# Optimization experiments

Hardware: AMD Instinct MI355X
Metric: run time of the kernel (lower is better)

The kernel has to match this reference:

```python
import jax, jax.numpy as jnp
import numpy as np

OUT_FEATURES = 4096
IN_FEATURES = 16384
NNZ = 2_000_000
BATCH = 128


def setup_inputs() -> dict:
    key = jax.random.key(0)
    k1, k2, k3, k4, k5 = jax.random.split(key, 5)
    inputs = jax.random.normal(k1, (BATCH, IN_FEATURES), dtype=jnp.float32)
    # learned sparse weight values and bias (uniform init like reset_parameters)
    bound = 1.0 / (IN_FEATURES ** 0.5)
    values = jax.random.uniform(k2, (NNZ,), minval=-bound, maxval=bound, dtype=jnp.float32)
    bias = jax.random.uniform(k3, (OUT_FEATURES,), minval=-bound, maxval=bound, dtype=jnp.float32)
    # fixed COO connectivity: rows -> out_features, cols -> in_features
    rows = jax.random.randint(k4, (NNZ,), 0, OUT_FEATURES, dtype=jnp.int32)
    cols = jax.random.randint(k5, (NNZ,), 0, IN_FEATURES, dtype=jnp.int32)
    return {"inputs": inputs, "values": values, "bias": bias, "rows": rows, "cols": cols}


def reference(inputs, values, bias, rows, cols):
    # out[b, r] = sum_{k: rows[k]==r} values[k] * inputs[b, cols[k]]  (+ bias[r])
    # Gather input columns per nnz entry, scale, then scatter-add into output rows.
    contrib = inputs[:, cols] * values            # [B, nnz]
    out = jax.ops.segment_sum(contrib.T, rows, num_segments=OUT_FEATURES).T  # [B, out_features]
    return out + bias
```

## Files before the change

kernel.cpp:

```cpp
#include <hip/hip_runtime.h>
#include <hip/hip_fp16.h>

#define NNZ    2000000
#define BATCH  128
#define IN_F   16384
#define OUT_F  4096
#define NCH    1024
#define CHUNK  1956
#define NBK    1024
#define RPB    4
#define BK_CAP 2240

__device__ inline int mbcnt64(unsigned long long m) {
  return __builtin_amdgcn_mbcnt_hi((unsigned)(m >> 32),
         __builtin_amdgcn_mbcnt_lo((unsigned)m, 0));
}

__global__ __launch_bounds__(512)
void k_localsort(const int* __restrict__ rows, const int* __restrict__ cols,
                 const float* __restrict__ vals, int* __restrict__ desc,
                 int2* __restrict__ pairs) {
  __shared__ int2 stage[CHUNK];
  __shared__ int  h[NBK], cur[NBK];
  __shared__ int  wsums[8];
  const int t = threadIdx.x, c = blockIdx.x;
  const int lane = t & 63, w = t >> 6;
  const int base = c * CHUNK;
  const int n = min(CHUNK, NNZ - base);
  const int n4 = n >> 2;

  h[t] = 0; h[t + 512] = 0;
  __syncthreads();
  for (int i = t; i < n4; i += 512) {
    const int4 r4 = ((const int4*)(rows + base))[i];
    atomicAdd(&h[r4.x >> 2], 1);
    atomicAdd(&h[r4.y >> 2], 1);
    atomicAdd(&h[r4.z >> 2], 1);
    atomicAdd(&h[r4.w >> 2], 1);
  }
  __syncthreads();
  const int v0 = h[2 * t], v1 = h[2 * t + 1];
  const int sv = v0 + v1;
  int x = sv;
#pragma unroll
  for (int off = 1; off < 64; off <<= 1) { int y = __shfl_up(x, off); if (lane >= off) x += y; }
  if (lane == 63) wsums[w] = x;
  __syncthreads();
  int wex = 0;
#pragma unroll
  for (int j = 0; j < 8; ++j) { const int sj = wsums[j]; wex += (j < w) ? sj : 0; }
  const int excl = wex + x - sv;
  cur[2 * t] = excl;
  cur[2 * t + 1] = excl + v0;
  ((int2*)desc)[c * 512 + t] = make_int2((excl << 8) | v0, ((excl + v0) << 8) | v1);
  __syncthreads();
  for (int i = t; i < n4; i += 512) {
    const int4   r4 = ((const int4*)(rows + base))[i];
    const int4   c4 = ((const int4*)(cols + base))[i];
    const float4 f4 = ((const float4*)(vals + base))[i];
    int pos;
    pos = atomicAdd(&cur[r4.x >> 2], 1); stage[pos] = make_int2((r4.x << 14) | c4.x, __float_as_int(f4.x));
    pos = atomicAdd(&cur[r4.y >> 2], 1); stage[pos] = make_int2((r4.y << 14) | c4.y, __float_as_int(f4.y));
    pos = atomicAdd(&cur[r4.z >> 2], 1); stage[pos] = make_int2((r4.z << 14) | c4.z, __float_as_int(f4.z));
    pos = atomicAdd(&cur[r4.w >> 2], 1); stage[pos] = make_int2((r4.w << 14) | c4.w, __float_as_int(f4.w));
  }
  __syncthreads();
  const int nh = n >> 1;
  for (int j = t; j < nh; j += 512)
    ((int4*)(pairs + base))[j] = ((const int4*)stage)[j];
}

__global__ __launch_bounds__(256)
void k_dtr(const int* __restrict__ desc, int* __restrict__ descT) {
  __shared__ int tile[32][33];
  const int tx = threadIdx.x, ty = threadIdx.y;
  const int x0 = blockIdx.x * 32, y0 = blockIdx.y * 32;
#pragma unroll
  for (int j = 0; j < 32; j += 8)
    tile[ty + j][tx] = desc[(y0 + ty + j) * NBK + x0 + tx];
  __syncthreads();
#pragma unroll
  for (int j = 0; j < 32; j += 8)
    descT[(x0 + ty + j) * NCH + y0 + tx] = tile[tx][ty + j];
}

__global__ __launch_bounds__(256)
void k_cscan(const int* __restrict__ descT, unsigned* __restrict__ rdesc,
             int* __restrict__ btot) {
  const int t = threadIdx.x, lane = t & 63, w = t >> 6;
  const int b = blockIdx.x * 4 + w;
  int carry = 0;
#pragma unroll
  for (int j = 0; j < 16; ++j) {
    const int cc = j * 64 + lane;
    const unsigned d = (unsigned)descT[b * NCH + cc];
    const int len = (int)(d & 255u);
    int x = len;
#pragma unroll
    for (int off = 1; off < 64; off <<= 1) { int y = __shfl_up(x, off); if (lane >= off) x += y; }
    rdesc[b * NCH + cc] = (d << 12) | (unsigned)(carry + x - len);
    carry += __shfl(x, 63);
  }
  if (lane == 0) btot[b] = carry;
}

__global__ __launch_bounds__(256)
void k_transpose(const float* __restrict__ in, __half* __restrict__ inT) {
  __shared__ float tile[32][33];
  const int tx = threadIdx.x, ty = threadIdx.y;
  const int c0 = blockIdx.x * 32, b0 = blockIdx.y * 32;
#pragma unroll
  for (int j = 0; j < 32; j += 8)
    tile[ty + j][tx] = in[(b0 + ty + j) * IN_F + c0 + tx];
  __syncthreads();
#pragma unroll
  for (int j = 0; j < 32; j += 8)
    inT[(size_t)(c0 + ty + j) * BATCH + b0 + tx] = __float2half(tile[tx][ty + j]);
}

#define REFILL(SL, KK) do { \
    const int idx = (hh_ + 2 * (KK)) * 8 + 2 * g; \
    const bool vld = idx < nr; \
    const int i0_ = vld ? (s + idx) : 0; \
    uint4 pp = *((const uint4*)(sorted + i0_)); \
    if (!vld) { pp.y = 0u; pp.w = 0u; } \
    x##SL##0 = inT[(pp.x & 16383u) * 16 + q]; \
    x##SL##1 = inT[(pp.z & 16383u) * 16 + q]; \
    pv##SL = make_uint2(pp.y, pp.w); \
  } while (0)

#define FMAH(SL) do { \
    const __half2 hv0 = __float2half2_rn(__uint_as_float(pv##SL.x)); \
    const __half2 hv1 = __float2half2_rn(__uint_as_float(pv##SL.y)); \
    const __half2* h0 = (const __half2*)&x##SL##0; \
    const __half2* h1 = (const __half2*)&x##SL##1; \
    hac0 = __hfma2(hv0, h0[0], hac0); hac1 = __hfma2(hv0, h0[1], hac1); \
    hac2 = __hfma2(hv0, h0[2], hac2); hac3 = __hfma2(hv0, h0[3], hac3); \
    hac0 = __hfma2(hv1, h1[0], hac0); hac1 = __hfma2(hv1, h1[1], hac1); \
    hac2 = __hfma2(hv1, h1[2], hac2); hac3 = __hfma2(hv1, h1[3], hac3); \
  } while (0)

#define STAGE(SL, NEXTKK) do { FMAH(SL); REFILL(SL, NEXTKK); } while (0)

#define FLUSH() do { \
    float2 f0 = __half22float2(hac0), f1 = __half22float2(hac1); \
    float2 f2 = __half22float2(hac2), f3 = __half22float2(hac3); \
    a0 += f0.x; a1 += f0.y; a2 += f1.x; a3 += f1.y; \
    a4 += f2.x; a5 += f2.y; a6 += f3.x; a7 += f3.y; \
    hac0 = hz; hac1 = hz; hac2 = hz; hac3 = hz; \
  } while (0)

__global__ __launch_bounds__(512, 8)
void k_spmm(const uint4* __restrict__ inT, const int2* __restrict__ pairs,
            const unsigned* __restrict__ rdesc, const int* __restrict__ btot,
            const float* __restrict__ bias, float* __restrict__ out) {
  __shared__ __align__(16) int2 staging[BK_CAP];
  __shared__ __align__(16) int2 sorted[BK_CAP + 8];
  __shared__ int  exd[NCH];
  __shared__ int  wrun[32];
  __shared__ unsigned long long wmask[32];
  __shared__ int  wcnt[32];
  __shared__ int  lst[RPB + 1];
  const int t = threadIdx.x, b = blockIdx.x;
  const int w = t >> 6, lane = t & 63;
  const int n = min(btot[b], BK_CAP);
  const int nrnd = (n + 511) & ~511;

  exd[t] = (int)rdesc[b * NCH + t];
  exd[t + 512] = (int)rdesc[b * NCH + t + 512];
  __syncthreads();
  for (int i = t; i < n; i += 512) {
    int lo = 0, hi = NCH - 1;
#pragma unroll
    for (int st = 0; st < 10; ++st) {
      const int mid = (lo + hi + 1) >> 1;
      if ((exd[mid] & 4095) <= i) lo = mid; else hi = mid - 1;
    }
    const unsigned d = (unsigned)exd[lo];
    staging[i] = pairs[lo * CHUNK + (int)(d >> 20) + (i - (int)(d & 4095u))];
  }
  __syncthreads();

  int cnt = 0;
  for (int i = w * 64 + lane; i < nrnd; i += 512) {
    const bool valid = i < n;
    const int key = valid ? staging[i].x : 0;
    const int r4 = valid ? ((key >> 14) & 3) : 4;
    unsigned long long m[4];
#pragma unroll
    for (int r = 0; r < 4; ++r) m[r] = __ballot(r4 == r);
    if (lane < 4) cnt += __popcll(m[lane]);
  }
  if (lane < 4) wcnt[w * 4 + lane] = cnt;
  __syncthreads();

  if (w == 0 && lane < 32) {
    const int v = wcnt[lane];
    int x = v;
#pragma unroll
    for (int off = 4; off < 32; off <<= 1) { int y = __shfl_up(x, off); if (lane >= off) x += y; }
    const int exw = x - v;
    int lstr = 0, tpad = 0;
#pragma unroll
    for (int rr = 0; rr < 4; ++rr) {
      const int tr = __shfl(x, 28 + rr);
      const int trE = (tr + 1) & ~1;
      if ((lane & 3) > rr) lstr += trE;
      tpad += trE;
    }
    wrun[lane] = lstr + exw;
    if (lane < 4) lst[lane] = lstr;
    if (lane == 0) lst[RPB] = tpad;
    if (lane >= 28) {
      if (x & 1) sorted[lstr + x] = make_int2(0, 0);
    }
  }
  __syncthreads();

  for (int i = w * 64 + lane; i < nrnd; i += 512) {
    const bool valid = i < n;
    const int2 p = valid ? staging[i] : make_int2(0, 0);
    const int r4 = valid ? ((p.x >> 14) & 3) : 4;
    unsigned long long m[4];
#pragma unroll
    for (int r = 0; r < 4; ++r) m[r] = __ballot(r4 == r);
    if (lane < 4) wmask[w * 4 + lane] = m[lane];
    if (valid) {
      const int rank = wrun[w * 4 + r4] + mbcnt64(wmask[w * 4 + r4]);
      sorted[rank] = p;
    }
    if (lane < 4) wrun[w * 4 + lane] += __popcll(m[lane]);
  }
  __syncthreads();

  const int rloc = w >> 1, hh_ = w & 1;
  const int r = b * RPB + rloc;
  const int g = lane >> 4, q = lane & 15;
  const int s = lst[rloc];
  const int nr = lst[rloc + 1] - s;
  const int nsteps = (nr + 7) >> 3;
  const int K = (nsteps + 1) >> 1;
  const int K3 = ((K + 2) / 3) * 3;

  float a0 = 0.f, a1 = 0.f, a2 = 0.f, a3 = 0.f, a4 = 0.f, a5 = 0.f, a6 = 0.f, a7 = 0.f;
  const __half2 hz = __float2half2_rn(0.f);
  __half2 hac0 = hz, hac1 = hz, hac2 = hz, hac3 = hz;
  uint4 xA0, xA1, xB0, xB1, xC0, xC1;
  uint2 pvA, pvB, pvC;

  REFILL(A, 0);
  REFILL(B, 1);
  REFILL(C, 2);
  for (int kk = 0; kk < K3; kk += 3) {
    STAGE(A, kk + 3);
    STAGE(B, kk + 4);
    STAGE(C, kk + 5);
    FLUSH();
  }

  a0 += __shfl_xor(a0, 16); a0 += __shfl_xor(a0, 32);
  a1 += __shfl_xor(a1, 16); a1 += __shfl_xor(a1, 32);
  a2 += __shfl_xor(a2, 16); a2 += __shfl_xor(a2, 32);
  a3 += __shfl_xor(a3, 16); a3 += __shfl_xor(a3, 32);
  a4 += __shfl_xor(a4, 16); a4 += __shfl_xor(a4, 32);
  a5 += __shfl_xor(a5, 16); a5 += __shfl_xor(a5, 32);
  a6 += __shfl_xor(a6, 16); a6 += __shfl_xor(a6, 32);
  a7 += __shfl_xor(a7, 16); a7 += __shfl_xor(a7, 32);

  float (*part)[BATCH] = (float (*)[BATCH])staging;
  if (hh_ == 1 && g == 0) {
    const int o = q * 8;
    part[rloc][o + 0] = a0; part[rloc][o + 1] = a1;
    part[rloc][o + 2] = a2; part[rloc][o + 3] = a3;
    part[rloc][o + 4] = a4; part[rloc][o + 5] = a5;
    part[rloc][o + 6] = a6; part[rloc][o + 7] = a7;
  }
  __syncthreads();
  if (hh_ == 0 && g == 0) {
    const float bs_ = bias[r];
    const int o = q * 8;
    out[(o + 0) * OUT_F + r] = a0 + part[rloc][o + 0] + bs_;
    out[(o + 1) * OUT_F + r] = a1 + part[rloc][o + 1] + bs_;
    out[(o + 2) * OUT_F + r] = a2 + part[rloc][o + 2] + bs_;
    out[(o + 3) * OUT_F + r] = a3 + part[rloc][o + 3] + bs_;
    out[(o + 4) * OUT_F + r] = a4 + part[rloc][o + 4] + bs_;
    out[(o + 5) * OUT_F + r] = a5 + part[rloc][o + 5] + bs_;
    out[(o + 6) * OUT_F + r] = a6 + part[rloc][o + 6] + bs_;
    out[(o + 7) * OUT_F + r] = a7 + part[rloc][o + 7] + bs_;
  }
}

extern "C" void kernel_launch(void* const* d_in, const int* in_sizes, int n_in,
                              void* d_out, int out_size, void* d_ws, size_t ws_size,
                              hipStream_t stream) {
  const float* inputs = (const float*)d_in[0];
  const float* values = (const float*)d_in[1];
  const float* bias   = (const float*)d_in[2];
  const int*   rows   = (const int*)d_in[3];
  const int*   cols   = (const int*)d_in[4];
  float* out = (float*)d_out;

  char* ws = (char*)d_ws;
  __half*   inputT = (__half*)(ws);
  int2*     pairs  = (int2*)(ws + 4194304);
  int*      desc   = (int*)(ws + 20217856);
  int*      descT  = (int*)(ws + 24412160);
  unsigned* rdesc  = (unsigned*)descT;
  int*      btot   = (int*)(ws + 28606464);

  k_localsort<<<NCH,     512, 0, stream>>>(rows, cols, values, desc, pairs);
  k_dtr      <<<dim3(NBK / 32, NCH / 32), dim3(32, 8), 0, stream>>>(desc, descT);
  k_cscan    <<<NBK / 4, 256, 0, stream>>>(descT, rdesc, btot);
  k_transpose<<<dim3(IN_F / 32, BATCH / 32), dim3(32, 8), 0, stream>>>(inputs, inputT);
  k_spmm     <<<NBK,     512, 0, stream>>>((const uint4*)inputT, pairs, rdesc, btot, bias, out);
}
```

Before: 133.9 us.

## Pack sorted nnz entries into 32-bit words with fp16 values, halve chunk count

Each sorted nonzero is packed into one 32-bit word (14-bit column, 2-bit local row, fp16 value) instead of an 8-byte pair, halving the pairs buffer traffic and LDS staging size. The chunk count drops from 1024 to 512 with doubled chunk size, shrinking the descriptor transpose/scan and the binary search depth in the spmm kernel. The value is now rounded to fp16 when written rather than when used, so the numeric result is unchanged. The layout and offsets of every kernel are rewritten to match.

```diff
diff --git a/kernel.cpp b/kernel.cpp
--- a/kernel.cpp
+++ b/kernel.cpp
@@ -5,8 +5,8 @@
 #define BATCH  128
 #define IN_F   16384
 #define OUT_F  4096
-#define NCH    1024
-#define CHUNK  1956
+#define NCH    512
+#define CHUNK  3912
 #define NBK    1024
 #define RPB    4
 #define BK_CAP 2240
@@ -16,13 +16,14 @@
          __builtin_amdgcn_mbcnt_lo((unsigned)m, 0));
 }
 
+
 __global__ __launch_bounds__(512)
 void k_localsort(const int* __restrict__ rows, const int* __restrict__ cols,
                  const float* __restrict__ vals, int* __restrict__ desc,
-                 int2* __restrict__ pairs) {
-  __shared__ int2 stage[CHUNK];
-  __shared__ int  h[NBK], cur[NBK];
-  __shared__ int  wsums[8];
+                 unsigned* __restrict__ pairs) {
+  __shared__ unsigned stage[CHUNK];
+  __shared__ int h[NBK], cur[NBK];
+  __shared__ int wsums[8];
   const int t = threadIdx.x, c = blockIdx.x;
   const int lane = t & 63, w = t >> 6;
   const int base = c * CHUNK;
@@ -59,15 +60,18 @@
     const int4   c4 = ((const int4*)(cols + base))[i];
     const float4 f4 = ((const float4*)(vals + base))[i];
     int pos;
-    pos = atomicAdd(&cur[r4.x >> 2], 1); stage[pos] = make_int2((r4.x << 14) | c4.x, __float_as_int(f4.x));
-    pos = atomicAdd(&cur[r4.y >> 2], 1); stage[pos] = make_int2((r4.y << 14) | c4.y, __float_as_int(f4.y));
-    pos = atomicAdd(&cur[r4.z >> 2], 1); stage[pos] = make_int2((r4.z << 14) | c4.z, __float_as_int(f4.z));
-    pos = atomicAdd(&cur[r4.w >> 2], 1); stage[pos] = make_int2((r4.w << 14) | c4.w, __float_as_int(f4.w));
-  }
-  __syncthreads();
-  const int nh = n >> 1;
-  for (int j = t; j < nh; j += 512)
-    ((int4*)(pairs + base))[j] = ((const int4*)stage)[j];
+    pos = atomicAdd(&cur[r4.x >> 2], 1);
+    stage[pos] = ((unsigned)c4.x << 18) | ((unsigned)(r4.x & 3) << 16) | (unsigned)__half_as_ushort(__float2half(f4.x));
+    pos = atomicAdd(&cur[r4.y >> 2], 1);
+    stage[pos] = ((unsigned)c4.y << 18) | ((unsigned)(r4.y & 3) << 16) | (unsigned)__half_as_ushort(__float2half(f4.y));
+    pos = atomicAdd(&cur[r4.z >> 2], 1);
+    stage[pos] = ((unsigned)c4.z << 18) | ((unsigned)(r4.z & 3) << 16) | (unsigned)__half_as_ushort(__float2half(f4.z));
+    pos = atomicAdd(&cur[r4.w >> 2], 1);
+    stage[pos] = ((unsigned)c4.w << 18) | ((unsigned)(r4.w & 3) << 16) | (unsigned)__half_as_ushort(__float2half(f4.w));
+  }
+  __syncthreads();
+  for (int j = t; j < n4; j += 512)
+    ((uint4*)(pairs + base))[j] = ((const uint4*)stage)[j];
 }
 
 __global__ __launch_bounds__(256)
@@ -91,7 +95,7 @@
   const int b = blockIdx.x * 4 + w;
   int carry = 0;
 #pragma unroll
-  for (int j = 0; j < 16; ++j) {
+  for (int j = 0; j < 8; ++j) {
     const int cc = j * 64 + lane;
     const unsigned d = (unsigned)descT[b * NCH + cc];
     const int len = (int)(d & 255u);
@@ -122,16 +126,16 @@
     const int idx = (hh_ + 2 * (KK)) * 8 + 2 * g; \
     const bool vld = idx < nr; \
     const int i0_ = vld ? (s + idx) : 0; \
-    uint4 pp = *((const uint4*)(sorted + i0_)); \
-    if (!vld) { pp.y = 0u; pp.w = 0u; } \
-    x##SL##0 = inT[(pp.x & 16383u) * 16 + q]; \
-    x##SL##1 = inT[(pp.z & 16383u) * 16 + q]; \
-    pv##SL = make_uint2(pp.y, pp.w); \
+    uint2 pp = *((const uint2*)(sorted + i0_)); \
+    if (!vld) { pp.x &= 0xffff0000u; pp.y &= 0xffff0000u; } \
+    x##SL##0 = inT[(pp.x >> 18) * 16 + q]; \
+    x##SL##1 = inT[(pp.y >> 18) * 16 + q]; \
+    pv##SL = pp; \
   } while (0)
 
 #define FMAH(SL) do { \
-    const __half2 hv0 = __float2half2_rn(__uint_as_float(pv##SL.x)); \
-    const __half2 hv1 = __float2half2_rn(__uint_as_float(pv##SL.y)); \
+    const __half2 hv0 = __half2half2(__ushort_as_half((unsigned short)(pv##SL.x & 0xffffu))); \
+    const __half2 hv1 = __half2half2(__ushort_as_half((unsigned short)(pv##SL.y & 0xffffu))); \
     const __half2* h0 = (const __half2*)&x##SL##0; \
     const __half2* h1 = (const __half2*)&x##SL##1; \
     hac0 = __hfma2(hv0, h0[0], hac0); hac1 = __hfma2(hv0, h0[1], hac1); \
@@ -151,11 +155,11 @@
   } while (0)
 
 __global__ __launch_bounds__(512, 8)
-void k_spmm(const uint4* __restrict__ inT, const int2* __restrict__ pairs,
+void k_spmm(const uint4* __restrict__ inT, const unsigned* __restrict__ pairs,
             const unsigned* __restrict__ rdesc, const int* __restrict__ btot,
             const float* __restrict__ bias, float* __restrict__ out) {
-  __shared__ __align__(16) int2 staging[BK_CAP];
-  __shared__ __align__(16) int2 sorted[BK_CAP + 8];
+  __shared__ __align__(16) unsigned staging[BK_CAP];
+  __shared__ __align__(16) unsigned sorted[BK_CAP + 8];
   __shared__ int  exd[NCH];
   __shared__ int  wrun[32];
   __shared__ unsigned long long wmask[32];
@@ -166,13 +170,12 @@
   const int n = min(btot[b], BK_CAP);
   const int nrnd = (n + 511) & ~511;
 
-  exd[t] = (int)rdesc[b * NCH + t];
-  exd[t + 512] = (int)rdesc[b * NCH + t + 512];
+  if (t < NCH) exd[t] = (int)rdesc[b * NCH + t];
   __syncthreads();
   for (int i = t; i < n; i += 512) {
     int lo = 0, hi = NCH - 1;
 #pragma unroll
-    for (int st = 0; st < 10; ++st) {
+    for (int st = 0; st < 9; ++st) {
       const int mid = (lo + hi + 1) >> 1;
       if ((exd[mid] & 4095) <= i) lo = mid; else hi = mid - 1;
     }
@@ -184,8 +187,8 @@
   int cnt = 0;
   for (int i = w * 64 + lane; i < nrnd; i += 512) {
     const bool valid = i < n;
-    const int key = valid ? staging[i].x : 0;
-    const int r4 = valid ? ((key >> 14) & 3) : 4;
+    const unsigned key = valid ? staging[i] : 0u;
+    const int r4 = valid ? (int)((key >> 16) & 3u) : 4;
     unsigned long long m[4];
 #pragma unroll
     for (int r = 0; r < 4; ++r) m[r] = __ballot(r4 == r);
@@ -212,15 +215,15 @@
     if (lane < 4) lst[lane] = lstr;
     if (lane == 0) lst[RPB] = tpad;
     if (lane >= 28) {
-      if (x & 1) sorted[lstr + x] = make_int2(0, 0);
+      if (x & 1) sorted[lstr + x] = 0u;
     }
   }
   __syncthreads();
 
   for (int i = w * 64 + lane; i < nrnd; i += 512) {
     const bool valid = i < n;
-    const int2 p = valid ? staging[i] : make_int2(0, 0);
-    const int r4 = valid ? ((p.x >> 14) & 3) : 4;
+    const unsigned p = valid ? staging[i] : 0u;
+    const int r4 = valid ? (int)((p >> 16) & 3u) : 4;
     unsigned long long m[4];
 #pragma unroll
     for (int r = 0; r < 4; ++r) m[r] = __ballot(r4 == r);
@@ -302,11 +305,11 @@
 
   char* ws = (char*)d_ws;
   __half*   inputT = (__half*)(ws);
-  int2*     pairs  = (int2*)(ws + 4194304);
-  int*      desc   = (int*)(ws + 20217856);
-  int*      descT  = (int*)(ws + 24412160);
+  unsigned* pairs  = (unsigned*)(ws + 4194304);
+  int*      desc   = (int*)(ws + 12206080);
+  int*      descT  = (int*)(ws + 14303232);
   unsigned* rdesc  = (unsigned*)descT;
-  int*      btot   = (int*)(ws + 28606464);
+  int*      btot   = (int*)(ws + 16400384);
 
   k_localsort<<<NCH,     512, 0, stream>>>(rows, cols, values, desc, pairs);
   k_dtr      <<<dim3(NBK / 32, NCH / 32), dim3(32, 8), 0, stream>>>(desc, descT);
```

Result: faster. 123.3 us (-7.9%).
